# Kernel tuning notes

Measured on AMD Instinct MI355X. Metric: run time of the kernel, lower is better.

Reference implementation:

```python
import jax, jax.numpy as jnp
import numpy as np

B, T, D = 64, 2048, 256

def setup_inputs() -> dict:
    key = jax.random.key(0)
    k1, _ = jax.random.split(key)
    ts = jnp.arange(T, dtype=jnp.float32) * 0.01  # increasing time grid
    noise = jax.random.normal(k1, (B, T, D), dtype=jnp.float32)
    mu = jnp.zeros((D,), jnp.float32)
    log_kappa = jnp.full((D,), -0.7, jnp.float32)
    log_sigma = jnp.full((D,), -0.7, jnp.float32)
    return {"ts": ts, "noise": noise, "mu": mu, "log_kappa": log_kappa, "log_sigma": log_sigma}

def _A_Q(kappa, sigma, dt):
    # exact OU transition coefficients; dt: [T-1,1], kappa/sigma: [D] -> [T-1,D]
    A = jnp.exp(-kappa * dt)
    two_k_dt = 2.0 * kappa * dt
    small = (two_k_dt < 1e-6).astype(dt.dtype)
    Q_exact = sigma ** 2 * (1.0 - jnp.exp(-two_k_dt)) / jnp.maximum(2.0 * kappa, 1e-12)
    Q_taylor = sigma ** 2 * dt * (1.0 - kappa * dt + two_k_dt ** 2 / 6.0)
    Q = small * Q_taylor + (1.0 - small) * Q_exact
    return A, Q

def reference(ts, noise, mu, log_kappa, log_sigma):
    kappa = jax.nn.softplus(log_kappa) + 1e-6
    sigma = jax.nn.softplus(log_sigma) + 1e-6
    var0 = sigma ** 2 / (2.0 * kappa)                      # stationary variance [D]
    y0 = mu + noise[:, 0, :] * jnp.sqrt(var0)              # [B,D]
    dt = jnp.maximum(ts[1:] - ts[:-1], 1e-6)[:, None]      # [T-1,1]
    A, Q = _A_Q(kappa, sigma, dt)                          # [T-1,D]
    # mean = mu + A*(y-mu) = A*y + mu*(1-A); fold noise in ahead of the scan
    b = mu * (1.0 - A)                                     # [T-1,D]
    eps = jnp.swapaxes(noise[:, 1:, :], 0, 1) * jnp.sqrt(Q)[:, None, :]  # [T-1,B,D]

    def step(y, xs):
        A_k, b_k, e_k = xs
        y_new = A_k * y + b_k + e_k
        return y_new, y_new

    _, ys = jax.lax.scan(step, y0, (A, b, eps))            # [T-1,B,D]
    y = jnp.concatenate([y0[None], ys], axis=0)            # [T,B,D]
    return jnp.swapaxes(y, 0, 1)                           # [B,T,D]
```

## Files before the change

### kernel.cpp

```cpp
#include <hip/hip_runtime.h>
#include <math.h>

#define BB 64
#define TT 2048
#define DD 256
#define D4 64
#define SS 64
#define LL (TT / SS)
#define WPB 4
#define BPG (BB / WPB)

typedef float f4 __attribute__((ext_vector_type(4)));


__device__ __forceinline__ float softplus_f(float x) {
    return (x > 0.f) ? (x + log1pf(expf(-x))) : log1pf(expf(x));
}

struct P4 { f4 k, s2, r, mu; };
struct C4 { f4 A, bm, sQ; };
struct P1 { float k, s2, r; };
struct C1 { float A, bm, sQ; };

__device__ __forceinline__ P1 sp1(float lk, float ls) {
    P1 o;
    o.k = softplus_f(lk) + 1e-6f;
    float s = softplus_f(ls) + 1e-6f;
    o.s2 = s * s;
    o.r = o.s2 / fmaxf(2.f * o.k, 1e-12f);
    return o;
}

__device__ __forceinline__ P4 load_params4(const f4* __restrict__ mu4,
                                           const f4* __restrict__ lk4,
                                           const f4* __restrict__ ls4,
                                           int lane) {
    f4 lk = lk4[lane], ls = ls4[lane], mu = mu4[lane];
    P4 p;
    P1 a;
    a = sp1(lk.x, ls.x); p.k.x = a.k; p.s2.x = a.s2; p.r.x = a.r;
    a = sp1(lk.y, ls.y); p.k.y = a.k; p.s2.y = a.s2; p.r.y = a.r;
    a = sp1(lk.z, ls.z); p.k.z = a.k; p.s2.z = a.s2; p.r.z = a.r;
    a = sp1(lk.w, ls.w); p.k.w = a.k; p.s2.w = a.s2; p.r.w = a.r;
    p.mu = mu;
    return p;
}

__device__ __forceinline__ C1 ou_coeff(float dt, float kappa, float s2, float r,
                                       float mu) {
    C1 o;
    float e = kappa * dt;
    o.A = __expf(-e);
    float two = 2.f * e;
    float Qe = r * (1.f - o.A * o.A);
    float Qt = s2 * dt * fmaf(two * two, (1.f / 6.f), 1.f - e);
    float Q = (two < 1e-6f) ? Qt : Qe;
    o.sQ = sqrtf(Q);
    o.bm = mu * (1.f - o.A);
    return o;
}

__device__ __forceinline__ C4 coeff4(float dt, const P4& p) {
    C4 c;
    C1 o;
    o = ou_coeff(dt, p.k.x, p.s2.x, p.r.x, p.mu.x); c.A.x = o.A; c.bm.x = o.bm; c.sQ.x = o.sQ;
    o = ou_coeff(dt, p.k.y, p.s2.y, p.r.y, p.mu.y); c.A.y = o.A; c.bm.y = o.bm; c.sQ.y = o.sQ;
    o = ou_coeff(dt, p.k.z, p.s2.z, p.r.z, p.mu.z); c.A.z = o.A; c.bm.z = o.bm; c.sQ.z = o.sQ;
    o = ou_coeff(dt, p.k.w, p.s2.w, p.r.w, p.mu.w); c.A.w = o.A; c.bm.w = o.bm; c.sQ.w = o.sQ;
    return c;
}

__device__ __forceinline__ void ou_step4(const C4& cc, const f4 n, f4& y) {
    f4 cv = cc.sQ * n + cc.bm;
    y = cc.A * y + cv;
}

__device__ __forceinline__ f4 sqrt4(const f4 v) {
    f4 r;
    r.x = sqrtf(v.x); r.y = sqrtf(v.y); r.z = sqrtf(v.z); r.w = sqrtf(v.w);
    return r;
}

__global__ __launch_bounds__(256) void ou_pass1(
    const float* __restrict__ ts, const f4* __restrict__ noise4,
    const f4* __restrict__ mu4, const f4* __restrict__ lk4,
    const f4* __restrict__ ls4,
    f4* __restrict__ Pw, f4* __restrict__ Uw) {
    __shared__ float dts[LL];
    const int lane = threadIdx.x & 63;
    const int w = threadIdx.x >> 6;
    const int s = blockIdx.x / BPG;
    const int bg = blockIdx.x % BPG;
    const int b = bg * WPB + w;
    const int t0 = s * LL;

    if (threadIdx.x < LL) {
        int k = t0 + threadIdx.x;
        float dt = 1e-6f;
        if (k >= 1) dt = fmaxf(ts[k] - ts[k - 1], 1e-6f);
        dts[threadIdx.x] = dt;
    }
    __syncthreads();

    P4 p = load_params4(mu4, lk4, ls4, lane);
    const f4* np = noise4 + (size_t)b * TT * D4 + lane;

    f4 U = {0.f, 0.f, 0.f, 0.f};
    f4 P = {1.f, 1.f, 1.f, 1.f};
    int kstart = t0;
    if (s == 0) {
        f4 n0 = np[0];
        U = n0 * sqrt4(p.r) + p.mu;
        P = (f4){0.f, 0.f, 0.f, 0.f};
        kstart = 1;
    }

    float dtprev = -1.f;
    C4 cc;
#pragma unroll 4
    for (int k = kstart; k < t0 + LL; ++k) {
        float dt = dts[k - t0];
        f4 n = np[(size_t)k * D4];
        if (dt != dtprev) { cc = coeff4(dt, p); dtprev = dt; }
        ou_step4(cc, n, U);
        P *= cc.A;
    }

    size_t idx = ((size_t)s * BB + b) * D4 + lane;
    Pw[idx] = P;
    Uw[idx] = U;
}

__global__ __launch_bounds__(64) void ou_pass2(
    const f4* __restrict__ Pw, const f4* __restrict__ Uw,
    f4* __restrict__ Ys) {
    const int lane = threadIdx.x;
    const int b = blockIdx.x;
    const size_t stride = (size_t)BB * D4;
    const size_t i0 = (size_t)b * D4 + lane;

    f4 inc = Uw[i0];
#pragma unroll 8
    for (int s = 1; s < SS; ++s) {
        size_t idx = i0 + (size_t)s * stride;
        f4 Pv = Pw[idx];
        f4 Uv = Uw[idx];
        Ys[idx] = inc;
        inc = Pv * inc + Uv;
    }
}

__global__ __launch_bounds__(256) void ou_pass3(
    const float* __restrict__ ts, const f4* __restrict__ noise4,
    const f4* __restrict__ mu4, const f4* __restrict__ lk4,
    const f4* __restrict__ ls4,
    const f4* __restrict__ Ys, f4* __restrict__ out4) {
    __shared__ float dts[LL];
    const int lane = threadIdx.x & 63;
    const int w = threadIdx.x >> 6;
    const int s = blockIdx.x / BPG;
    const int bg = blockIdx.x % BPG;
    const int b = bg * WPB + w;
    const int t0 = s * LL;

    if (threadIdx.x < LL) {
        int k = t0 + threadIdx.x;
        float dt = 1e-6f;
        if (k >= 1) dt = fmaxf(ts[k] - ts[k - 1], 1e-6f);
        dts[threadIdx.x] = dt;
    }
    __syncthreads();

    P4 p = load_params4(mu4, lk4, ls4, lane);
    const f4* np = noise4 + (size_t)b * TT * D4 + lane;
    f4* op = out4 + (size_t)b * TT * D4 + lane;

    f4 y;
    int kstart = t0;
    if (s == 0) {
        f4 n0 = np[0];
        y = n0 * sqrt4(p.r) + p.mu;
        __builtin_nontemporal_store(y, op);
        kstart = 1;
    } else {
        y = Ys[((size_t)s * BB + b) * D4 + lane];
    }

    float dtprev = -1.f;
    C4 cc;
#pragma unroll 4
    for (int k = kstart; k < t0 + LL; ++k) {
        float dt = dts[k - t0];
        f4 n = np[(size_t)k * D4];
        if (dt != dtprev) { cc = coeff4(dt, p); dtprev = dt; }
        ou_step4(cc, n, y);
        __builtin_nontemporal_store(y, op + (size_t)k * D4);
    }
}

__global__ __launch_bounds__(128) void ou_fallback(
    const float* __restrict__ ts, const float2* __restrict__ noise2,
    const float2* __restrict__ mu2, const float2* __restrict__ lk2,
    const float2* __restrict__ ls2, float2* __restrict__ out2) {
    __shared__ float dts[TT];
    const int tid = threadIdx.x;
    const int b = blockIdx.x;
    for (int i = tid; i < TT; i += 128) {
        float dt = 1e-6f;
        if (i >= 1) dt = fmaxf(ts[i] - ts[i - 1], 1e-6f);
        dts[i] = dt;
    }
    __syncthreads();

    float2 lk = lk2[tid], ls = ls2[tid], mu = mu2[tid];
    P1 px = sp1(lk.x, ls.x);
    P1 py = sp1(lk.y, ls.y);

    const float2* np = noise2 + (size_t)b * TT * 128 + tid;
    float2* op = out2 + (size_t)b * TT * 128 + tid;

    float2 n0 = np[0];
    float2 y;
    y.x = fmaf(n0.x, sqrtf(px.r), mu.x);
    y.y = fmaf(n0.y, sqrtf(py.r), mu.y);
    op[0] = y;

#pragma unroll 4
    for (int k = 1; k < TT; ++k) {
        float dt = dts[k];
        float2 n = np[(size_t)k * 128];
        C1 cx = ou_coeff(dt, px.k, px.s2, px.r, mu.x);
        C1 cy = ou_coeff(dt, py.k, py.s2, py.r, mu.y);
        y.x = fmaf(cx.A, y.x, fmaf(cx.sQ, n.x, cx.bm));
        y.y = fmaf(cy.A, y.y, fmaf(cy.sQ, n.y, cy.bm));
        op[(size_t)k * 128] = y;
    }
}

extern "C" void kernel_launch(void* const* d_in, const int* in_sizes, int n_in,
                              void* d_out, int out_size, void* d_ws, size_t ws_size,
                              hipStream_t stream) {
    const float* ts = (const float*)d_in[0];
    const f4* noise4 = (const f4*)d_in[1];
    const f4* mu4 = (const f4*)d_in[2];
    const f4* lk4 = (const f4*)d_in[3];
    const f4* ls4 = (const f4*)d_in[4];
    f4* out4 = (f4*)d_out;

    const size_t seg = (size_t)SS * BB * D4;
    if (ws_size >= 3 * seg * sizeof(f4)) {
        f4* Pw = (f4*)d_ws;
        f4* Uw = Pw + seg;
        f4* Ys = Uw + seg;
        ou_pass1<<<SS * BPG, 256, 0, stream>>>(ts, noise4, mu4, lk4, ls4, Pw, Uw);
        ou_pass2<<<BB, 64, 0, stream>>>(Pw, Uw, Ys);
        ou_pass3<<<SS * BPG, 256, 0, stream>>>(ts, noise4, mu4, lk4, ls4, Ys, out4);
    } else {
        ou_fallback<<<BB, 128, 0, stream>>>(ts, (const float2*)d_in[1],
                                            (const float2*)d_in[2],
                                            (const float2*)d_in[3],
                                            (const float2*)d_in[4],
                                            (float2*)d_out);
    }
}
```

Before: 90.52 us.

## Fuse three-pass chunked scan into one cooperative kernel with grid syncs

```diff
diff --git a/kernel.cpp b/kernel.cpp
--- a/kernel.cpp
+++ b/kernel.cpp
@@ -1,5 +1,8 @@
 #include <hip/hip_runtime.h>
+#include <hip/hip_cooperative_groups.h>
 #include <math.h>
+
+namespace cg = cooperative_groups;
 
 #define BB 64
 #define TT 2048
@@ -9,6 +12,8 @@
 #define LL (TT / SS)
 #define WPB 4
 #define BPG (BB / WPB)
+#define GRID (SS * BPG)
+#define SCAN_BLOCKS ((BB * D4) / 256)
 
 typedef float f4 __attribute__((ext_vector_type(4)));
 
@@ -81,6 +86,104 @@
     return r;
 }
 
+__global__ __launch_bounds__(256, 4) void ou_fused(
+    const float* __restrict__ ts, const f4* __restrict__ noise4,
+    const f4* __restrict__ mu4, const f4* __restrict__ lk4,
+    const f4* __restrict__ ls4,
+    f4* __restrict__ Pw, f4* __restrict__ Uw, f4* __restrict__ Ys,
+    f4* __restrict__ out4) {
+    cg::grid_group grid = cg::this_grid();
+    __shared__ float dts[LL];
+    const int lane = threadIdx.x & 63;
+    const int w = threadIdx.x >> 6;
+    const int s = blockIdx.x / BPG;
+    const int bg = blockIdx.x % BPG;
+    const int b = bg * WPB + w;
+    const int t0 = s * LL;
+
+    if (threadIdx.x < LL) {
+        int k = t0 + threadIdx.x;
+        float dt = 1e-6f;
+        if (k >= 1) dt = fmaxf(ts[k] - ts[k - 1], 1e-6f);
+        dts[threadIdx.x] = dt;
+    }
+    __syncthreads();
+
+    P4 p = load_params4(mu4, lk4, ls4, lane);
+    const f4* np = noise4 + (size_t)b * TT * D4 + lane;
+    const size_t myidx = ((size_t)s * BB + b) * D4 + lane;
+
+    {
+        f4 U = {0.f, 0.f, 0.f, 0.f};
+        f4 P = {1.f, 1.f, 1.f, 1.f};
+        int kstart = t0;
+        if (s == 0) {
+            f4 n0 = np[0];
+            U = n0 * sqrt4(p.r) + p.mu;
+            P = (f4){0.f, 0.f, 0.f, 0.f};
+            kstart = 1;
+        }
+        float dtprev = -1.f;
+        C4 cc;
+#pragma unroll 4
+        for (int k = kstart; k < t0 + LL; ++k) {
+            float dt = dts[k - t0];
+            f4 n = np[(size_t)k * D4];
+            if (dt != dtprev) { cc = coeff4(dt, p); dtprev = dt; }
+            ou_step4(cc, n, U);
+            P *= cc.A;
+        }
+        Pw[myidx] = P;
+        Uw[myidx] = U;
+    }
+
+    grid.sync();
+
+    if (blockIdx.x < SCAN_BLOCKS) {
+        const int gt = blockIdx.x * 256 + threadIdx.x;
+        const int b2 = gt >> 6;
+        const int l2 = gt & 63;
+        const size_t stride = (size_t)BB * D4;
+        const size_t i0 = (size_t)b2 * D4 + l2;
+        f4 inc = Uw[i0];
+#pragma unroll 8
+        for (int s2 = 1; s2 < SS; ++s2) {
+            size_t idx = i0 + (size_t)s2 * stride;
+            f4 Pv = Pw[idx];
+            f4 Uv = Uw[idx];
+            Ys[idx] = inc;
+            inc = Pv * inc + Uv;
+        }
+    }
+
+    grid.sync();
+
+    {
+        f4* op = out4 + (size_t)b * TT * D4 + lane;
+        f4 y;
+        int kstart = t0;
+        if (s == 0) {
+            f4 n0 = np[0];
+            y = n0 * sqrt4(p.r) + p.mu;
+            __builtin_nontemporal_store(y, op);
+            kstart = 1;
+        } else {
+            y = Ys[myidx];
+        }
+        float dtprev = -1.f;
+        C4 cc;
+#pragma unroll 4
+        for (int k = kstart; k < t0 + LL; ++k) {
+            float dt = dts[k - t0];
+            f4 n = np[(size_t)k * D4];
+            if (dt != dtprev) { cc = coeff4(dt, p); dtprev = dt; }
+            ou_step4(cc, n, y);
+            __builtin_nontemporal_store(y, op + (size_t)k * D4);
+        }
+    }
+}
+
+
 __global__ __launch_bounds__(256) void ou_pass1(
     const float* __restrict__ ts, const f4* __restrict__ noise4,
     const f4* __restrict__ mu4, const f4* __restrict__ lk4,
@@ -248,13 +351,39 @@
     f4* out4 = (f4*)d_out;
 
     const size_t seg = (size_t)SS * BB * D4;
-    if (ws_size >= 3 * seg * sizeof(f4)) {
+    const bool have_ws = ws_size >= 3 * seg * sizeof(f4);
+
+    if (have_ws) {
         f4* Pw = (f4*)d_ws;
         f4* Uw = Pw + seg;
         f4* Ys = Uw + seg;
-        ou_pass1<<<SS * BPG, 256, 0, stream>>>(ts, noise4, mu4, lk4, ls4, Pw, Uw);
+
+        static int coop_ok = -1;
+        if (coop_ok < 0) {
+            int nb = 0, ncu = 0, dev = 0;
+            hipError_t e1 = hipGetDevice(&dev);
+            hipError_t e2 = hipOccupancyMaxActiveBlocksPerMultiprocessor(
+                &nb, reinterpret_cast<const void*>(&ou_fused), 256, 0);
+            hipError_t e3 = hipDeviceGetAttribute(
+                &ncu, hipDeviceAttributeMultiprocessorCount, dev);
+            coop_ok = (e1 == hipSuccess && e2 == hipSuccess && e3 == hipSuccess &&
+                       (long)nb * ncu >= GRID) ? 1 : 0;
+        }
+
+        if (coop_ok) {
+            void* args[] = {(void*)&ts, (void*)&noise4, (void*)&mu4, (void*)&lk4,
+                            (void*)&ls4, (void*)&Pw, (void*)&Uw, (void*)&Ys,
+                            (void*)&out4};
+            hipError_t le = hipLaunchCooperativeKernel(
+                reinterpret_cast<const void*>(&ou_fused), dim3(GRID), dim3(256),
+                args, 0, stream);
+            if (le == hipSuccess) return;
+            (void)hipGetLastError();
+        }
+
+        ou_pass1<<<GRID, 256, 0, stream>>>(ts, noise4, mu4, lk4, ls4, Pw, Uw);
         ou_pass2<<<BB, 64, 0, stream>>>(Pw, Uw, Ys);
-        ou_pass3<<<SS * BPG, 256, 0, stream>>>(ts, noise4, mu4, lk4, ls4, Ys, out4);
+        ou_pass3<<<GRID, 256, 0, stream>>>(ts, noise4, mu4, lk4, ls4, Ys, out4);
     } else {
         ou_fallback<<<BB, 128, 0, stream>>>(ts, (const float2*)d_in[1],
                                             (const float2*)d_in[2],
```

Result: no change. 90.52 us (-0.0%).

## Write local scan output in first pass and apply linear boundary correction

Applied to the files above, without the earlier changes.

```diff
diff --git a/kernel.cpp b/kernel.cpp
--- a/kernel.cpp
+++ b/kernel.cpp
@@ -3,7 +3,6 @@
 
 #define BB 64
 #define TT 2048
-#define DD 256
 #define D4 64
 #define SS 64
 #define LL (TT / SS)
@@ -70,22 +69,17 @@
     return c;
 }
 
-__device__ __forceinline__ void ou_step4(const C4& cc, const f4 n, f4& y) {
-    f4 cv = cc.sQ * n + cc.bm;
-    y = cc.A * y + cv;
-}
-
 __device__ __forceinline__ f4 sqrt4(const f4 v) {
     f4 r;
     r.x = sqrtf(v.x); r.y = sqrtf(v.y); r.z = sqrtf(v.z); r.w = sqrtf(v.w);
     return r;
 }
 
-__global__ __launch_bounds__(256) void ou_pass1(
+__global__ __launch_bounds__(256) void ou_local(
     const float* __restrict__ ts, const f4* __restrict__ noise4,
     const f4* __restrict__ mu4, const f4* __restrict__ lk4,
     const f4* __restrict__ ls4,
-    f4* __restrict__ Pw, f4* __restrict__ Uw) {
+    f4* __restrict__ Pw, f4* __restrict__ Uw, f4* __restrict__ out4) {
     __shared__ float dts[LL];
     const int lane = threadIdx.x & 63;
     const int w = threadIdx.x >> 6;
@@ -104,14 +98,16 @@
 
     P4 p = load_params4(mu4, lk4, ls4, lane);
     const f4* np = noise4 + (size_t)b * TT * D4 + lane;
-
-    f4 U = {0.f, 0.f, 0.f, 0.f};
+    f4* op = out4 + (size_t)b * TT * D4 + lane;
+
+    f4 y = {0.f, 0.f, 0.f, 0.f};
     f4 P = {1.f, 1.f, 1.f, 1.f};
     int kstart = t0;
     if (s == 0) {
-        f4 n0 = np[0];
-        U = n0 * sqrt4(p.r) + p.mu;
+        f4 n0 = __builtin_nontemporal_load(np);
+        y = n0 * sqrt4(p.r) + p.mu;
         P = (f4){0.f, 0.f, 0.f, 0.f};
+        op[0] = y;
         kstart = 1;
     }
 
@@ -120,18 +116,20 @@
 #pragma unroll 4
     for (int k = kstart; k < t0 + LL; ++k) {
         float dt = dts[k - t0];
-        f4 n = np[(size_t)k * D4];
+        f4 n = __builtin_nontemporal_load(np + (size_t)k * D4);
         if (dt != dtprev) { cc = coeff4(dt, p); dtprev = dt; }
-        ou_step4(cc, n, U);
+        f4 cv = cc.sQ * n + cc.bm;
+        y = cc.A * y + cv;
         P *= cc.A;
+        op[(size_t)k * D4] = y;
     }
 
     size_t idx = ((size_t)s * BB + b) * D4 + lane;
     Pw[idx] = P;
-    Uw[idx] = U;
-}
-
-__global__ __launch_bounds__(64) void ou_pass2(
+    Uw[idx] = y;
+}
+
+__global__ __launch_bounds__(64) void ou_bound(
     const f4* __restrict__ Pw, const f4* __restrict__ Uw,
     f4* __restrict__ Ys) {
     const int lane = threadIdx.x;
@@ -150,51 +148,50 @@
     }
 }
 
-__global__ __launch_bounds__(256) void ou_pass3(
-    const float* __restrict__ ts, const f4* __restrict__ noise4,
-    const f4* __restrict__ mu4, const f4* __restrict__ lk4,
-    const f4* __restrict__ ls4,
+__global__ __launch_bounds__(256) void ou_correct(
+    const float* __restrict__ ts, const f4* __restrict__ lk4,
     const f4* __restrict__ Ys, f4* __restrict__ out4) {
     __shared__ float dts[LL];
     const int lane = threadIdx.x & 63;
     const int w = threadIdx.x >> 6;
-    const int s = blockIdx.x / BPG;
+    const int s = (SS - 1) - (blockIdx.x / BPG);
     const int bg = blockIdx.x % BPG;
     const int b = bg * WPB + w;
     const int t0 = s * LL;
 
     if (threadIdx.x < LL) {
         int k = t0 + threadIdx.x;
-        float dt = 1e-6f;
-        if (k >= 1) dt = fmaxf(ts[k] - ts[k - 1], 1e-6f);
-        dts[threadIdx.x] = dt;
+        dts[threadIdx.x] = fmaxf(ts[k] - ts[k - 1], 1e-6f);
     }
     __syncthreads();
 
-    P4 p = load_params4(mu4, lk4, ls4, lane);
-    const f4* np = noise4 + (size_t)b * TT * D4 + lane;
+    f4 lk = lk4[lane];
+    f4 kap;
+    kap.x = softplus_f(lk.x) + 1e-6f;
+    kap.y = softplus_f(lk.y) + 1e-6f;
+    kap.z = softplus_f(lk.z) + 1e-6f;
+    kap.w = softplus_f(lk.w) + 1e-6f;
+
+    const f4 ystart = Ys[((size_t)s * BB + b) * D4 + lane];
     f4* op = out4 + (size_t)b * TT * D4 + lane;
 
-    f4 y;
-    int kstart = t0;
-    if (s == 0) {
-        f4 n0 = np[0];
-        y = n0 * sqrt4(p.r) + p.mu;
-        __builtin_nontemporal_store(y, op);
-        kstart = 1;
-    } else {
-        y = Ys[((size_t)s * BB + b) * D4 + lane];
-    }
-
+    f4 prefix = {1.f, 1.f, 1.f, 1.f};
     float dtprev = -1.f;
-    C4 cc;
+    f4 A;
 #pragma unroll 4
-    for (int k = kstart; k < t0 + LL; ++k) {
-        float dt = dts[k - t0];
-        f4 n = np[(size_t)k * D4];
-        if (dt != dtprev) { cc = coeff4(dt, p); dtprev = dt; }
-        ou_step4(cc, n, y);
-        __builtin_nontemporal_store(y, op + (size_t)k * D4);
+    for (int i = 0; i < LL; ++i) {
+        float dt = dts[i];
+        if (dt != dtprev) {
+            A.x = __expf(-kap.x * dt);
+            A.y = __expf(-kap.y * dt);
+            A.z = __expf(-kap.z * dt);
+            A.w = __expf(-kap.w * dt);
+            dtprev = dt;
+        }
+        prefix *= A;
+        f4 yh = op[(size_t)(t0 + i) * D4];
+        f4 y = prefix * ystart + yh;
+        __builtin_nontemporal_store(y, op + (size_t)(t0 + i) * D4);
     }
 }
 
@@ -252,9 +249,10 @@
         f4* Pw = (f4*)d_ws;
         f4* Uw = Pw + seg;
         f4* Ys = Uw + seg;
-        ou_pass1<<<SS * BPG, 256, 0, stream>>>(ts, noise4, mu4, lk4, ls4, Pw, Uw);
-        ou_pass2<<<BB, 64, 0, stream>>>(Pw, Uw, Ys);
-        ou_pass3<<<SS * BPG, 256, 0, stream>>>(ts, noise4, mu4, lk4, ls4, Ys, out4);
+        ou_local<<<SS * BPG, 256, 0, stream>>>(ts, noise4, mu4, lk4, ls4,
+                                               Pw, Uw, out4);
+        ou_bound<<<BB, 64, 0, stream>>>(Pw, Uw, Ys);
+        ou_correct<<<(SS - 1) * BPG, 256, 0, stream>>>(ts, lk4, Ys, out4);
     } else {
         ou_fallback<<<BB, 128, 0, stream>>>(ts, (const float2*)d_in[1],
                                             (const float2*)d_in[2],
```

Measured after the change: 112.7 us. +24.5%, slower.
